# Performance work log

Measured on AMD Instinct MI355X. Metric: run time of the kernel, lower is better.

Reference implementation:

```python
import jax, jax.numpy as jnp
import numpy as np

NEG_SLOPE = 0.2  # PyG GATv2Conv default negative_slope


def gatv2_layer(x, src, dst, n, Wl, bl, Wr, br, att, bias):
    """GATv2Conv with heads=1, concat=False, add aggregation.
    src -> dst edges; softmax normalized per destination node."""
    xl = x @ Wl + bl            # source-side transform  [N, C]
    xr = x @ Wr + br            # target-side transform  [N, C]
    m = jax.nn.leaky_relu(xl[src] + xr[dst], NEG_SLOPE)  # [E, C]
    e = m @ att                 # attention logits [E]
    emax = jax.ops.segment_max(e, dst, num_segments=n)
    emax = jnp.where(jnp.isfinite(emax), emax, 0.0)  # guard isolated nodes
    ex = jnp.exp(e - emax[dst])
    denom = jax.ops.segment_sum(ex, dst, num_segments=n)
    alpha = ex / denom[dst]     # ragged per-node softmax [E]
    out = jax.ops.segment_sum(alpha[:, None] * xl[src], dst, num_segments=n)
    return out + bias


def setup_inputs() -> dict:
    key = jax.random.key(0)
    ks = jax.random.split(key, 16)
    N, E = 50000, 800000
    C_in, C_h, C_out = 1, 256, 128

    def lin(k, fan_in, fan_out):
        s = (1.0 / np.sqrt(fan_in)).astype(np.float32) if isinstance(fan_in, np.ndarray) else 1.0 / np.sqrt(fan_in)
        return jax.random.normal(k, (fan_in, fan_out), dtype=jnp.float32) * s

    inp = {
        "x": jax.random.normal(ks[0], (N, C_in), dtype=jnp.float32),
        "edge_index": jax.random.randint(ks[1], (2, E), 0, N, dtype=jnp.int32),
        # layer 1 (1 -> 256)
        "Wl1": lin(ks[2], C_in, C_h),
        "bl1": jnp.zeros((C_h,), jnp.float32),
        "Wr1": lin(ks[3], C_in, C_h),
        "br1": jnp.zeros((C_h,), jnp.float32),
        "att1": jax.random.normal(ks[4], (C_h,), dtype=jnp.float32) / np.sqrt(C_h),
        "bias1": jnp.zeros((C_h,), jnp.float32),
        # PReLU (per-channel, init 0.25 like torch)
        "prelu_w": jnp.full((C_h,), 0.25, jnp.float32),
        # layer 2 (256 -> 128)
        "Wl2": lin(ks[5], C_h, C_out),
        "bl2": jnp.zeros((C_out,), jnp.float32),
        "Wr2": lin(ks[6], C_h, C_out),
        "br2": jnp.zeros((C_out,), jnp.float32),
        "att2": jax.random.normal(ks[7], (C_out,), dtype=jnp.float32) / np.sqrt(C_out),
        "bias2": jnp.zeros((C_out,), jnp.float32),
    }
    return inp


def reference(x, edge_index, Wl1, bl1, Wr1, br1, att1, bias1, prelu_w,
              Wl2, bl2, Wr2, br2, att2, bias2):
    n = x.shape[0]
    # PyG GATv2Conv default add_self_loops=True
    loops = jnp.arange(n, dtype=edge_index.dtype)
    src = jnp.concatenate([edge_index[0], loops])
    dst = jnp.concatenate([edge_index[1], loops])

    h = gatv2_layer(x, src, dst, n, Wl1, bl1, Wr1, br1, att1, bias1)
    h = jnp.where(h > 0, h, prelu_w * h)  # PReLU(hidden_channels)
    out = gatv2_layer(h, src, dst, n, Wl2, bl2, Wr2, br2, att2, bias2)
    return out
```

## Files before the change

kernel.cpp:

```cpp
#include <hip/hip_runtime.h>
#include <hip/hip_bf16.h>

#define SLOPE 0.2f

typedef __attribute__((ext_vector_type(8))) short short8;
typedef __attribute__((ext_vector_type(4))) float f32x4;

static __device__ __forceinline__ unsigned short f2bf(float f) {
  __hip_bfloat16 h = __float2bfloat16(f);
  return *reinterpret_cast<unsigned short*>(&h);
}

static __device__ __forceinline__ void packedReduce4(
    float q0, float q1, float q2, float q3,
    float& p0, float& p1, float& p2, float& p3) {
  int lane = threadIdx.x & 63;
  float u = (lane & 1) ? q1 : q0;
  float v = (lane & 1) ? q0 : q1;
  u += __shfl_xor(v, 1, 64);
  float w = (lane & 1) ? q3 : q2;
  float z = (lane & 1) ? q2 : q3;
  w += __shfl_xor(z, 1, 64);
  float a = (lane & 2) ? w : u;
  float b = (lane & 2) ? u : w;
  a += __shfl_xor(b, 2, 64);
  a += __shfl_xor(a, 4, 64);
  a += __shfl_xor(a, 8, 64);
  a += __shfl_xor(a, 16, 64);
  a += __shfl_xor(a, 32, 64);
  p0 = __shfl(a, 0, 64);
  p1 = __shfl(a, 1, 64);
  p2 = __shfl(a, 2, 64);
  p3 = __shfl(a, 3, 64);
}

__global__ void count_kernel(const int* __restrict__ ei, int E, int N, int* __restrict__ deg) {
  int t = blockIdx.x * blockDim.x + threadIdx.x;
  int Etot = E + N;
  int j0 = t * 8;
  if (j0 >= Etot) return;
  if (j0 + 8 <= E) {
    int4 a = *(const int4*)(ei + E + j0);
    int4 b = *(const int4*)(ei + E + j0 + 4);
    atomicAdd(&deg[a.x], 1); atomicAdd(&deg[a.y], 1);
    atomicAdd(&deg[a.z], 1); atomicAdd(&deg[a.w], 1);
    atomicAdd(&deg[b.x], 1); atomicAdd(&deg[b.y], 1);
    atomicAdd(&deg[b.z], 1); atomicAdd(&deg[b.w], 1);
  } else {
#pragma unroll
    for (int i = 0; i < 8; ++i) {
      int j = j0 + i;
      if (j < Etot) {
        int d = (j < E) ? ei[E + j] : (j - E);
        atomicAdd(&deg[d], 1);
      }
    }
  }
}

__global__ __launch_bounds__(1024) void scan1_kernel(const int* __restrict__ deg, int N,
                                                     int* __restrict__ bsum) {
  __shared__ int ws[16];
  int i = blockIdx.x * 1024 + threadIdx.x;
  int v = (i < N) ? deg[i] : 0;
#pragma unroll
  for (int off = 32; off > 0; off >>= 1) v += __shfl_xor(v, off, 64);
  int wave = threadIdx.x >> 6;
  if ((threadIdx.x & 63) == 0) ws[wave] = v;
  __syncthreads();
  if (threadIdx.x == 0) {
    int s = 0;
#pragma unroll
    for (int k = 0; k < 16; ++k) s += ws[k];
    bsum[blockIdx.x] = s;
  }
}

__global__ __launch_bounds__(1024) void scan2_kernel(const int* __restrict__ bsum, int B,
                                                     int* __restrict__ boff) {
  __shared__ int s[1024];
  int tid = threadIdx.x;
  s[tid] = (tid < B) ? bsum[tid] : 0;
  __syncthreads();
  for (int off = 1; off < 1024; off <<= 1) {
    int t = (tid >= off) ? s[tid - off] : 0;
    __syncthreads();
    s[tid] += t;
    __syncthreads();
  }
  if (tid < B) boff[tid] = (tid == 0) ? 0 : s[tid - 1];
}

__global__ __launch_bounds__(1024) void scan3_kernel(const int* __restrict__ deg,
                                                     const int* __restrict__ boff, int N,
                                                     int* __restrict__ rowptr,
                                                     int* __restrict__ cursor) {
  __shared__ int s[1024];
  int tid = threadIdx.x;
  int i = blockIdx.x * 1024 + tid;
  int v = (i < N) ? deg[i] : 0;
  s[tid] = v;
  __syncthreads();
  for (int off = 1; off < 1024; off <<= 1) {
    int t = (tid >= off) ? s[tid - off] : 0;
    __syncthreads();
    s[tid] += t;
    __syncthreads();
  }
  int base = boff[blockIdx.x];
  if (i < N) {
    int excl = base + s[tid] - v;
    rowptr[i] = excl;
    cursor[i] = excl;
    if (i == N - 1) rowptr[N] = base + s[tid];
  }
}

__global__ void scatter_kernel(const int* __restrict__ ei, int E, int N,
                               int* __restrict__ cursor, int* __restrict__ srcs) {
  int t = blockIdx.x * blockDim.x + threadIdx.x;
  int Etot = E + N;
  int j0 = t * 8;
  if (j0 >= Etot) return;
  if (j0 + 8 <= E) {
    int4 sa = *(const int4*)(ei + j0);
    int4 sb = *(const int4*)(ei + j0 + 4);
    int4 da = *(const int4*)(ei + E + j0);
    int4 db = *(const int4*)(ei + E + j0 + 4);
    int p0 = atomicAdd(&cursor[da.x], 1);
    int p1 = atomicAdd(&cursor[da.y], 1);
    int p2 = atomicAdd(&cursor[da.z], 1);
    int p3 = atomicAdd(&cursor[da.w], 1);
    int p4 = atomicAdd(&cursor[db.x], 1);
    int p5 = atomicAdd(&cursor[db.y], 1);
    int p6 = atomicAdd(&cursor[db.z], 1);
    int p7 = atomicAdd(&cursor[db.w], 1);
    srcs[p0] = sa.x; srcs[p1] = sa.y; srcs[p2] = sa.z; srcs[p3] = sa.w;
    srcs[p4] = sb.x; srcs[p5] = sb.y; srcs[p6] = sb.z; srcs[p7] = sb.w;
  } else {
#pragma unroll
    for (int i = 0; i < 8; ++i) {
      int j = j0 + i;
      if (j < Etot) {
        int s, d;
        if (j < E) { s = ei[j]; d = ei[E + j]; } else { s = j - E; d = j - E; }
        int pos = atomicAdd(&cursor[d], 1);
        srcs[pos] = s;
      }
    }
  }
}

__global__ void l1const_kernel(const float* __restrict__ Wl1, const float* __restrict__ bl1,
                               const float* __restrict__ Wr1, const float* __restrict__ br1,
                               const float* __restrict__ att1, float* __restrict__ agd) {
  int lane = threadIdx.x & 63;
  int c0 = lane * 4;
  float4 wl = *(const float4*)(Wl1 + c0);
  float4 wr = *(const float4*)(Wr1 + c0);
  float4 ba = *(const float4*)(bl1 + c0);
  float4 bb = *(const float4*)(br1 + c0);
  float4 at = *(const float4*)(att1 + c0);
  float pa = at.x * wl.x + at.y * wl.y + at.z * wl.z + at.w * wl.w;
  float pg = at.x * wr.x + at.y * wr.y + at.z * wr.z + at.w * wr.w;
  float pd = at.x * (ba.x + bb.x) + at.y * (ba.y + bb.y) +
             at.z * (ba.z + bb.z) + at.w * (ba.w + bb.w);
#pragma unroll
  for (int off = 32; off > 0; off >>= 1) {
    pa += __shfl_xor(pa, off, 64);
    pg += __shfl_xor(pg, off, 64);
    pd += __shfl_xor(pd, off, 64);
  }
  if (lane == 0) { agd[0] = pa; agd[1] = pg; agd[2] = pd; }
}

__global__ __launch_bounds__(256) void l1_fused_kernel(
    const float* __restrict__ x, const int* __restrict__ srcs,
    const int* __restrict__ rowptr, int N,
    const float* __restrict__ Wl1, const float* __restrict__ bl1,
    const float* __restrict__ Wr1, const float* __restrict__ br1,
    const float* __restrict__ att1, const float* __restrict__ agd,
    float* __restrict__ S1) {
  int wid = (blockIdx.x * blockDim.x + threadIdx.x) >> 6;
  int lane = threadIdx.x & 63;
  if (wid >= N) return;
  int c0 = lane * 4;
  float4 wl = *(const float4*)(Wl1 + c0);
  float4 wr = *(const float4*)(Wr1 + c0);
  float4 ba = *(const float4*)(bl1 + c0);
  float4 bb = *(const float4*)(br1 + c0);
  float4 at = *(const float4*)(att1 + c0);
  float xd = x[wid];
  float cc0 = fmaf(xd, wr.x, ba.x + bb.x);
  float cc1 = fmaf(xd, wr.y, ba.y + bb.y);
  float cc2 = fmaf(xd, wr.z, ba.z + bb.z);
  float cc3 = fmaf(xd, wr.w, ba.w + bb.w);
  float a40 = 0.4f * at.x, a41 = 0.4f * at.y, a42 = 0.4f * at.z, a43 = 0.4f * at.w;
  float alpha = agd[0], gamma = agd[1], delta = agd[2];
  float beta = fmaf(xd, gamma, delta);
  float al6 = 0.6f * alpha, be6 = 0.6f * beta;

  int base = rowptr[wid], end = rowptr[wid + 1];
  float m = -INFINITY, S = 0.f, vs = 0.f;
  for (int k0 = base; k0 < end; k0 += 4) {
    int k1 = min(k0 + 1, end - 1);
    int k2 = min(k0 + 2, end - 1);
    int k3 = min(k0 + 3, end - 1);
    float xs0 = x[srcs[k0]];
    float xs1 = x[srcs[k1]];
    float xs2 = x[srcs[k2]];
    float xs3 = x[srcs[k3]];

    float q0, q1, q2, q3;
    {
      float z0, z1, z2, z3;
#define L1ABS(xs, q)                                                      \
      z0 = fmaf(xs, wl.x, cc0); z1 = fmaf(xs, wl.y, cc1);                 \
      z2 = fmaf(xs, wl.z, cc2); z3 = fmaf(xs, wl.w, cc3);                 \
      q = fmaf(fabsf(z0), a40, fmaf(fabsf(z1), a41,                       \
            fmaf(fabsf(z2), a42, fabsf(z3) * a43)));
      L1ABS(xs0, q0) L1ABS(xs1, q1) L1ABS(xs2, q2) L1ABS(xs3, q3)
#undef L1ABS
    }
    float p0, p1, p2, p3;
    packedReduce4(q0, q1, q2, q3, p0, p1, p2, p3);
    p0 += fmaf(xs0, al6, be6);
    p1 += fmaf(xs1, al6, be6);
    p2 += fmaf(xs2, al6, be6);
    p3 += fmaf(xs3, al6, be6);
    if (k0 + 1 >= end) p1 = -INFINITY;
    if (k0 + 2 >= end) p2 = -INFINITY;
    if (k0 + 3 >= end) p3 = -INFINITY;

    float pmax = fmaxf(fmaxf(p0, p1), fmaxf(p2, p3));
    if (pmax > m) {
      float sc = __expf(m - pmax);
      S *= sc; vs *= sc;
      m = pmax;
    }
    float w0 = __expf(p0 - m), w1 = __expf(p1 - m);
    float w2 = __expf(p2 - m), w3 = __expf(p3 - m);
    S += (w0 + w1) + (w2 + w3);
    vs += fmaf(w0, xs0, fmaf(w1, xs1, fmaf(w2, xs2, w3 * xs3)));
  }
  if (lane == 0) S1[wid] = vs / S;
}

__global__ __launch_bounds__(1024) void wcvt_kernel(
    const float* __restrict__ Wl2, const float* __restrict__ Wr2,
    __hip_bfloat16* __restrict__ Wt) {
  __shared__ float tile[32][33];
  int k0 = blockIdx.y * 32, c0 = blockIdx.x * 32;
  int tx = threadIdx.x & 31, ty = threadIdx.x >> 5;
  int k = k0 + ty, c = c0 + tx;
  float v = (c < 128) ? Wl2[(size_t)k * 128 + c] : Wr2[(size_t)k * 128 + (c - 128)];
  tile[ty][tx] = v;
  __syncthreads();
  Wt[(size_t)(c0 + ty) * 256 + k0 + tx] = __float2bfloat16(tile[tx][ty]);
}

__global__ __launch_bounds__(512) void l2_transform_mfma(
    const float* __restrict__ S1,
    const float* __restrict__ Wl1, const float* __restrict__ bl1,
    const float* __restrict__ bias1, const float* __restrict__ prelu_w,
    const __hip_bfloat16* __restrict__ Wt,
    const float* __restrict__ bl2, const float* __restrict__ br2,
    int N, unsigned short* __restrict__ xl2b, unsigned short* __restrict__ xr2b) {
  int w = threadIdx.x >> 6;
  int lane = threadIdx.x & 63;
  int l15 = lane & 15, lk = lane >> 4;
  int rbase = blockIdx.x * 128 + (w & 1) * 64;
  int cbase = (w >> 1) * 64;

  float s1v[4];
#pragma unroll
  for (int mt = 0; mt < 4; ++mt) {
    int r = rbase + mt * 16 + l15;
    s1v[mt] = (r < N) ? S1[r] : 0.f;
  }

  f32x4 acc[4][4] = {};

#pragma unroll
  for (int ks = 0; ks < 8; ++ks) {
    int k0 = ks * 32 + lk * 8;
    float4 wl1a = *(const float4*)(Wl1 + k0);
    float4 wl1b = *(const float4*)(Wl1 + k0 + 4);
    float4 b1a  = *(const float4*)(bl1 + k0);
    float4 b1b  = *(const float4*)(bl1 + k0 + 4);
    float4 z1a  = *(const float4*)(bias1 + k0);
    float4 z1b  = *(const float4*)(bias1 + k0 + 4);
    float4 pwa  = *(const float4*)(prelu_w + k0);
    float4 pwb  = *(const float4*)(prelu_w + k0 + 4);
    float wv[8] = {wl1a.x, wl1a.y, wl1a.z, wl1a.w, wl1b.x, wl1b.y, wl1b.z, wl1b.w};
    float cv[8] = {b1a.x + z1a.x, b1a.y + z1a.y, b1a.z + z1a.z, b1a.w + z1a.w,
                   b1b.x + z1b.x, b1b.y + z1b.y, b1b.z + z1b.z, b1b.w + z1b.w};
    float pv[8] = {pwa.x, pwa.y, pwa.z, pwa.w, pwb.x, pwb.y, pwb.z, pwb.w};

    short8 afrag[4];
#pragma unroll
    for (int mt = 0; mt < 4; ++mt) {
      short8 a;
#pragma unroll
      for (int j = 0; j < 8; ++j) {
        float t = fmaf(wv[j], s1v[mt], cv[j]);
        t = (t > 0.f) ? t : pv[j] * t;
        a[j] = (short)f2bf(t);
      }
      afrag[mt] = a;
    }

    short8 bfrag[4];
#pragma unroll
    for (int nt = 0; nt < 4; ++nt) {
      int col = cbase + nt * 16 + l15;
      bfrag[nt] = *(const short8*)(Wt + (size_t)col * 256 + k0);
    }

#pragma unroll
    for (int mt = 0; mt < 4; ++mt)
#pragma unroll
      for (int nt = 0; nt < 4; ++nt)
        acc[mt][nt] = __builtin_amdgcn_mfma_f32_16x16x32_bf16(afrag[mt], bfrag[nt],
                                                              acc[mt][nt], 0, 0, 0);
  }

#pragma unroll
  for (int mt = 0; mt < 4; ++mt) {
#pragma unroll
    for (int nt = 0; nt < 4; ++nt) {
      int col = cbase + nt * 16 + l15;
      float bias;
      unsigned short* dst;
      int cc;
      if (col < 128) { bias = bl2[col]; dst = xl2b; cc = col; }
      else           { bias = br2[col - 128]; dst = xr2b; cc = col - 128; }
#pragma unroll
      for (int r = 0; r < 4; ++r) {
        int row = rbase + mt * 16 + lk * 4 + r;
        if (row < N) dst[(size_t)row * 128 + cc] = f2bf(acc[mt][nt][r] + bias);
      }
    }
  }
}

__global__ __launch_bounds__(256) void l2_fused_kernel(
    const unsigned short* __restrict__ xl2b, const unsigned short* __restrict__ xr2b,
    const int* __restrict__ srcs, const int* __restrict__ rowptr,
    const float* __restrict__ att2, const float* __restrict__ bias2,
    int N, float* __restrict__ out) {
  int wid = (blockIdx.x * blockDim.x + threadIdx.x) >> 6;
  int lane = threadIdx.x & 63;
  if (wid >= N) return;
  unsigned c0 = (unsigned)(lane * 2);
  float2 at = *(const float2*)(att2 + c0);
  unsigned qd = *(const unsigned*)(xr2b + (((unsigned)wid << 7) + c0));
  float drx = __uint_as_float(qd << 16);
  float dry = __uint_as_float(qd & 0xffff0000u);
  int base = rowptr[wid], end = rowptr[wid + 1];
  float m = -INFINITY, S = 0.f, a0 = 0.f, a1 = 0.f;
  for (int k0 = base; k0 < end; k0 += 4) {
    int k1 = min(k0 + 1, end - 1);
    int k2 = min(k0 + 2, end - 1);
    int k3 = min(k0 + 3, end - 1);
    unsigned s0 = (unsigned)srcs[k0], s1 = (unsigned)srcs[k1];
    unsigned s2 = (unsigned)srcs[k2], s3 = (unsigned)srcs[k3];
    unsigned q0 = *(const unsigned*)(xl2b + ((s0 << 7) + c0));
    unsigned q1 = *(const unsigned*)(xl2b + ((s1 << 7) + c0));
    unsigned q2 = *(const unsigned*)(xl2b + ((s2 << 7) + c0));
    unsigned q3 = *(const unsigned*)(xl2b + ((s3 << 7) + c0));
    float r0x = __uint_as_float(q0 << 16), r0y = __uint_as_float(q0 & 0xffff0000u);
    float r1x = __uint_as_float(q1 << 16), r1y = __uint_as_float(q1 & 0xffff0000u);
    float r2x = __uint_as_float(q2 << 16), r2y = __uint_as_float(q2 & 0xffff0000u);
    float r3x = __uint_as_float(q3 << 16), r3y = __uint_as_float(q3 & 0xffff0000u);

    float e0, e1, e2, e3;
    {
      float v0, v1;
#define L2DOT(rx, ry, q)                                        \
      v0 = rx + drx; v0 = fmaxf(v0, SLOPE * v0);                \
      v1 = ry + dry; v1 = fmaxf(v1, SLOPE * v1);                \
      q = fmaf(v0, at.x, v1 * at.y);
      L2DOT(r0x, r0y, e0) L2DOT(r1x, r1y, e1) L2DOT(r2x, r2y, e2) L2DOT(r3x, r3y, e3)
#undef L2DOT
    }
    float p0, p1, p2, p3;
    packedReduce4(e0, e1, e2, e3, p0, p1, p2, p3);
    if (k0 + 1 >= end) p1 = -INFINITY;
    if (k0 + 2 >= end) p2 = -INFINITY;
    if (k0 + 3 >= end) p3 = -INFINITY;

    float pmax = fmaxf(fmaxf(p0, p1), fmaxf(p2, p3));
    if (pmax > m) {
      float sc = __expf(m - pmax);
      S *= sc; a0 *= sc; a1 *= sc;
      m = pmax;
    }
    float w0 = __expf(p0 - m), w1 = __expf(p1 - m);
    float w2 = __expf(p2 - m), w3 = __expf(p3 - m);
    S += (w0 + w1) + (w2 + w3);
    a0 += fmaf(w0, r0x, fmaf(w1, r1x, fmaf(w2, r2x, w3 * r3x)));
    a1 += fmaf(w0, r0y, fmaf(w1, r1y, fmaf(w2, r2y, w3 * r3y)));
  }
  float inv = 1.f / S;
  float2 bz = *(const float2*)(bias2 + c0);
  float2 res;
  res.x = fmaf(a0, inv, bz.x);
  res.y = fmaf(a1, inv, bz.y);
  *(float2*)(out + (((unsigned)wid << 7) + c0)) = res;
}

extern "C" void kernel_launch(void* const* d_in, const int* in_sizes, int n_in,
                              void* d_out, int out_size, void* d_ws, size_t ws_size,
                              hipStream_t stream) {
  const float* x      = (const float*)d_in[0];
  const int*   ei     = (const int*)d_in[1];
  const float* Wl1    = (const float*)d_in[2];
  const float* bl1    = (const float*)d_in[3];
  const float* Wr1    = (const float*)d_in[4];
  const float* br1    = (const float*)d_in[5];
  const float* att1   = (const float*)d_in[6];
  const float* bias1  = (const float*)d_in[7];
  const float* prelu  = (const float*)d_in[8];
  const float* Wl2    = (const float*)d_in[9];
  const float* bl2    = (const float*)d_in[10];
  const float* Wr2    = (const float*)d_in[11];
  const float* br2    = (const float*)d_in[12];
  const float* att2   = (const float*)d_in[13];
  const float* bias2  = (const float*)d_in[14];
  float* out = (float*)d_out;

  int N = in_sizes[0];
  int E = in_sizes[1] / 2;
  int Etot = E + N;

  char* ws = (char*)d_ws;
  size_t off = 0;
  auto alloc = [&](size_t bytes) -> void* {
    void* p = ws + off;
    off = (off + bytes + 255) & ~(size_t)255;
    return p;
  };
  float* S1     = (float*)alloc((size_t)N * 4);
  unsigned short* xl2b = (unsigned short*)alloc((size_t)N * 128 * 2);
  unsigned short* xr2b = (unsigned short*)alloc((size_t)N * 128 * 2);
  int*   deg    = (int*)alloc((size_t)N * 4);
  int*   rowptr = (int*)alloc((size_t)(N + 1) * 4);
  int*   cursor = (int*)alloc((size_t)N * 4);
  int*   srcs   = (int*)alloc((size_t)Etot * 4);
  int*   bsum   = (int*)alloc((size_t)1024 * 4);
  int*   boff   = (int*)alloc((size_t)1024 * 4);
  float* agd    = (float*)alloc((size_t)16 * 4);
  __hip_bfloat16* Wt = (__hip_bfloat16*)alloc((size_t)256 * 256 * 2);
  (void)ws_size; (void)n_in; (void)out_size;

  hipMemsetAsync(deg, 0, (size_t)N * 4, stream);

  int B = (N + 1023) / 1024;
  int g8 = (Etot + 8 * 256 - 1) / (8 * 256);
  count_kernel<<<g8, 256, 0, stream>>>(ei, E, N, deg);
  scan1_kernel<<<B, 1024, 0, stream>>>(deg, N, bsum);
  scan2_kernel<<<1, 1024, 0, stream>>>(bsum, B, boff);
  scan3_kernel<<<B, 1024, 0, stream>>>(deg, boff, N, rowptr, cursor);
  scatter_kernel<<<g8, 256, 0, stream>>>(ei, E, N, cursor, srcs);

  l1const_kernel<<<1, 64, 0, stream>>>(Wl1, bl1, Wr1, br1, att1, agd);
  wcvt_kernel<<<dim3(8, 8), 1024, 0, stream>>>(Wl2, Wr2, Wt);

  l1_fused_kernel<<<(N + 3) / 4, 256, 0, stream>>>(x, srcs, rowptr, N,
                                                   Wl1, bl1, Wr1, br1, att1, agd, S1);
  l2_transform_mfma<<<(N + 127) / 128, 512, 0, stream>>>(S1, Wl1, bl1, bias1, prelu,
                                                         Wt, bl2, br2, N, xl2b, xr2b);
  l2_fused_kernel<<<(N + 3) / 4, 256, 0, stream>>>(xl2b, xr2b, srcs, rowptr,
                                                   att2, bias2, N, out);
}
```

Before: 313.2 us.

## Record per-edge rank during degree count to drop scatter atomics; merge const kernel

The degree-count kernel now stores the value returned by each atomicAdd as a per-edge rank. The scatter kernel then places each source at rowptr[dst]+rank with no atomics, and the cursor array goes away. The tiny layer-1 constant kernel is merged into the weight-conversion kernel to save one launch. In exchange it adds a rank array of E+N ints that is written once and read back, plus a gather of rowptr in the scatter.

Result: faster. 281.6 us (-10.1%).

```diff
diff --git a/kernel.cpp b/kernel.cpp
--- a/kernel.cpp
+++ b/kernel.cpp
@@ -34,7 +34,8 @@
   p3 = __shfl(a, 3, 64);
 }
 
-__global__ void count_kernel(const int* __restrict__ ei, int E, int N, int* __restrict__ deg) {
+__global__ void count_kernel(const int* __restrict__ ei, int E, int N,
+                             int* __restrict__ deg, int* __restrict__ rank) {
   int t = blockIdx.x * blockDim.x + threadIdx.x;
   int Etot = E + N;
   int j0 = t * 8;
@@ -42,17 +43,20 @@
   if (j0 + 8 <= E) {
     int4 a = *(const int4*)(ei + E + j0);
     int4 b = *(const int4*)(ei + E + j0 + 4);
-    atomicAdd(&deg[a.x], 1); atomicAdd(&deg[a.y], 1);
-    atomicAdd(&deg[a.z], 1); atomicAdd(&deg[a.w], 1);
-    atomicAdd(&deg[b.x], 1); atomicAdd(&deg[b.y], 1);
-    atomicAdd(&deg[b.z], 1); atomicAdd(&deg[b.w], 1);
+    int4 ra, rb;
+    ra.x = atomicAdd(&deg[a.x], 1); ra.y = atomicAdd(&deg[a.y], 1);
+    ra.z = atomicAdd(&deg[a.z], 1); ra.w = atomicAdd(&deg[a.w], 1);
+    rb.x = atomicAdd(&deg[b.x], 1); rb.y = atomicAdd(&deg[b.y], 1);
+    rb.z = atomicAdd(&deg[b.z], 1); rb.w = atomicAdd(&deg[b.w], 1);
+    *(int4*)(rank + j0) = ra;
+    *(int4*)(rank + j0 + 4) = rb;
   } else {
 #pragma unroll
     for (int i = 0; i < 8; ++i) {
       int j = j0 + i;
       if (j < Etot) {
         int d = (j < E) ? ei[E + j] : (j - E);
-        atomicAdd(&deg[d], 1);
+        rank[j] = atomicAdd(&deg[d], 1);
       }
     }
   }
@@ -93,8 +97,7 @@
 
 __global__ __launch_bounds__(1024) void scan3_kernel(const int* __restrict__ deg,
                                                      const int* __restrict__ boff, int N,
-                                                     int* __restrict__ rowptr,
-                                                     int* __restrict__ cursor) {
+                                                     int* __restrict__ rowptr) {
   __shared__ int s[1024];
   int tid = threadIdx.x;
   int i = blockIdx.x * 1024 + tid;
@@ -109,15 +112,14 @@
   }
   int base = boff[blockIdx.x];
   if (i < N) {
-    int excl = base + s[tid] - v;
-    rowptr[i] = excl;
-    cursor[i] = excl;
+    rowptr[i] = base + s[tid] - v;
     if (i == N - 1) rowptr[N] = base + s[tid];
   }
 }
 
-__global__ void scatter_kernel(const int* __restrict__ ei, int E, int N,
-                               int* __restrict__ cursor, int* __restrict__ srcs) {
+__global__ void scatter_kernel(const int* __restrict__ ei, const int* __restrict__ rank,
+                               const int* __restrict__ rowptr, int E, int N,
+                               int* __restrict__ srcs) {
   int t = blockIdx.x * blockDim.x + threadIdx.x;
   int Etot = E + N;
   int j0 = t * 8;
@@ -127,16 +129,16 @@
     int4 sb = *(const int4*)(ei + j0 + 4);
     int4 da = *(const int4*)(ei + E + j0);
     int4 db = *(const int4*)(ei + E + j0 + 4);
-    int p0 = atomicAdd(&cursor[da.x], 1);
-    int p1 = atomicAdd(&cursor[da.y], 1);
-    int p2 = atomicAdd(&cursor[da.z], 1);
-    int p3 = atomicAdd(&cursor[da.w], 1);
-    int p4 = atomicAdd(&cursor[db.x], 1);
-    int p5 = atomicAdd(&cursor[db.y], 1);
-    int p6 = atomicAdd(&cursor[db.z], 1);
-    int p7 = atomicAdd(&cursor[db.w], 1);
-    srcs[p0] = sa.x; srcs[p1] = sa.y; srcs[p2] = sa.z; srcs[p3] = sa.w;
-    srcs[p4] = sb.x; srcs[p5] = sb.y; srcs[p6] = sb.z; srcs[p7] = sb.w;
+    int4 ra = *(const int4*)(rank + j0);
+    int4 rb = *(const int4*)(rank + j0 + 4);
+    srcs[rowptr[da.x] + ra.x] = sa.x;
+    srcs[rowptr[da.y] + ra.y] = sa.y;
+    srcs[rowptr[da.z] + ra.z] = sa.z;
+    srcs[rowptr[da.w] + ra.w] = sa.w;
+    srcs[rowptr[db.x] + rb.x] = sb.x;
+    srcs[rowptr[db.y] + rb.y] = sb.y;
+    srcs[rowptr[db.z] + rb.z] = sb.z;
+    srcs[rowptr[db.w] + rb.w] = sb.w;
   } else {
 #pragma unroll
     for (int i = 0; i < 8; ++i) {
@@ -144,34 +146,47 @@
       if (j < Etot) {
         int s, d;
         if (j < E) { s = ei[j]; d = ei[E + j]; } else { s = j - E; d = j - E; }
-        int pos = atomicAdd(&cursor[d], 1);
-        srcs[pos] = s;
+        srcs[rowptr[d] + rank[j]] = s;
       }
     }
   }
 }
 
-__global__ void l1const_kernel(const float* __restrict__ Wl1, const float* __restrict__ bl1,
-                               const float* __restrict__ Wr1, const float* __restrict__ br1,
-                               const float* __restrict__ att1, float* __restrict__ agd) {
-  int lane = threadIdx.x & 63;
-  int c0 = lane * 4;
-  float4 wl = *(const float4*)(Wl1 + c0);
-  float4 wr = *(const float4*)(Wr1 + c0);
-  float4 ba = *(const float4*)(bl1 + c0);
-  float4 bb = *(const float4*)(br1 + c0);
-  float4 at = *(const float4*)(att1 + c0);
-  float pa = at.x * wl.x + at.y * wl.y + at.z * wl.z + at.w * wl.w;
-  float pg = at.x * wr.x + at.y * wr.y + at.z * wr.z + at.w * wr.w;
-  float pd = at.x * (ba.x + bb.x) + at.y * (ba.y + bb.y) +
-             at.z * (ba.z + bb.z) + at.w * (ba.w + bb.w);
-#pragma unroll
-  for (int off = 32; off > 0; off >>= 1) {
-    pa += __shfl_xor(pa, off, 64);
-    pg += __shfl_xor(pg, off, 64);
-    pd += __shfl_xor(pd, off, 64);
-  }
-  if (lane == 0) { agd[0] = pa; agd[1] = pg; agd[2] = pd; }
+__global__ __launch_bounds__(1024) void wcvt_kernel(
+    const float* __restrict__ Wl2, const float* __restrict__ Wr2,
+    __hip_bfloat16* __restrict__ Wt,
+    const float* __restrict__ Wl1, const float* __restrict__ bl1,
+    const float* __restrict__ Wr1, const float* __restrict__ br1,
+    const float* __restrict__ att1, float* __restrict__ agd) {
+  __shared__ float tile[32][33];
+  int k0 = blockIdx.y * 32, c0 = blockIdx.x * 32;
+  int tx = threadIdx.x & 31, ty = threadIdx.x >> 5;
+  int k = k0 + ty, c = c0 + tx;
+  float v = (c < 128) ? Wl2[(size_t)k * 128 + c] : Wr2[(size_t)k * 128 + (c - 128)];
+  tile[ty][tx] = v;
+  __syncthreads();
+  Wt[(size_t)(c0 + ty) * 256 + k0 + tx] = __float2bfloat16(tile[tx][ty]);
+
+  if (blockIdx.x == 0 && blockIdx.y == 0 && threadIdx.x < 64) {
+    int lane = threadIdx.x;
+    int cc = lane * 4;
+    float4 wl = *(const float4*)(Wl1 + cc);
+    float4 wr = *(const float4*)(Wr1 + cc);
+    float4 ba = *(const float4*)(bl1 + cc);
+    float4 bb = *(const float4*)(br1 + cc);
+    float4 at = *(const float4*)(att1 + cc);
+    float pa = at.x * wl.x + at.y * wl.y + at.z * wl.z + at.w * wl.w;
+    float pg = at.x * wr.x + at.y * wr.y + at.z * wr.z + at.w * wr.w;
+    float pd = at.x * (ba.x + bb.x) + at.y * (ba.y + bb.y) +
+               at.z * (ba.z + bb.z) + at.w * (ba.w + bb.w);
+#pragma unroll
+    for (int off = 32; off > 0; off >>= 1) {
+      pa += __shfl_xor(pa, off, 64);
+      pg += __shfl_xor(pg, off, 64);
+      pd += __shfl_xor(pd, off, 64);
+    }
+    if (lane == 0) { agd[0] = pa; agd[1] = pg; agd[2] = pd; }
+  }
 }
 
 __global__ __launch_bounds__(256) void l1_fused_kernel(
@@ -244,19 +259,6 @@
     vs += fmaf(w0, xs0, fmaf(w1, xs1, fmaf(w2, xs2, w3 * xs3)));
   }
   if (lane == 0) S1[wid] = vs / S;
-}
-
-__global__ __launch_bounds__(1024) void wcvt_kernel(
-    const float* __restrict__ Wl2, const float* __restrict__ Wr2,
-    __hip_bfloat16* __restrict__ Wt) {
-  __shared__ float tile[32][33];
-  int k0 = blockIdx.y * 32, c0 = blockIdx.x * 32;
-  int tx = threadIdx.x & 31, ty = threadIdx.x >> 5;
-  int k = k0 + ty, c = c0 + tx;
-  float v = (c < 128) ? Wl2[(size_t)k * 128 + c] : Wr2[(size_t)k * 128 + (c - 128)];
-  tile[ty][tx] = v;
-  __syncthreads();
-  Wt[(size_t)(c0 + ty) * 256 + k0 + tx] = __float2bfloat16(tile[tx][ty]);
 }
 
 __global__ __launch_bounds__(512) void l2_transform_mfma(
@@ -446,7 +448,7 @@
   unsigned short* xr2b = (unsigned short*)alloc((size_t)N * 128 * 2);
   int*   deg    = (int*)alloc((size_t)N * 4);
   int*   rowptr = (int*)alloc((size_t)(N + 1) * 4);
-  int*   cursor = (int*)alloc((size_t)N * 4);
+  int*   rank   = (int*)alloc((size_t)Etot * 4);
   int*   srcs   = (int*)alloc((size_t)Etot * 4);
   int*   bsum   = (int*)alloc((size_t)1024 * 4);
   int*   boff   = (int*)alloc((size_t)1024 * 4);
@@ -458,14 +460,14 @@
 
   int B = (N + 1023) / 1024;
   int g8 = (Etot + 8 * 256 - 1) / (8 * 256);
-  count_kernel<<<g8, 256, 0, stream>>>(ei, E, N, deg);
+  count_kernel<<<g8, 256, 0, stream>>>(ei, E, N, deg, rank);
   scan1_kernel<<<B, 1024, 0, stream>>>(deg, N, bsum);
   scan2_kernel<<<1, 1024, 0, stream>>>(bsum, B, boff);
-  scan3_kernel<<<B, 1024, 0, stream>>>(deg, boff, N, rowptr, cursor);
-  scatter_kernel<<<g8, 256, 0, stream>>>(ei, E, N, cursor, srcs);
-
-  l1const_kernel<<<1, 64, 0, stream>>>(Wl1, bl1, Wr1, br1, att1, agd);
-  wcvt_kernel<<<dim3(8, 8), 1024, 0, stream>>>(Wl2, Wr2, Wt);
+  scan3_kernel<<<B, 1024, 0, stream>>>(deg, boff, N, rowptr);
+  scatter_kernel<<<g8, 256, 0, stream>>>(ei, rank, rowptr, E, N, srcs);
+
+  wcvt_kernel<<<dim3(8, 8), 1024, 0, stream>>>(Wl2, Wr2, Wt,
+                                               Wl1, bl1, Wr1, br1, att1, agd);
 
   l1_fused_kernel<<<(N + 3) / 4, 256, 0, stream>>>(x, srcs, rowptr, N,
                                                    Wl1, bl1, Wr1, br1, att1, agd, S1);
```
